# Optimization experiments

Measured on AMD Instinct MI355X. Metric: run time of the kernel, lower is better.

## Reference

```python
import jax, jax.numpy as jnp
import numpy as np

D = 64          # embedding_dim
B = 1024        # batch (queries)
R = 128         # num_relations
N = 100000      # num_nodes
E = 6400000     # num_edges


def setup_inputs() -> dict:
    key = jax.random.key(0)
    ks = jax.random.split(key, 16)
    inp = {
        "relation_embeddings": jax.random.normal(ks[0], (B, R, D), dtype=jnp.float32),
        "query_rels": jax.random.randint(ks[1], (B,), 0, R),
        "query_entities": jax.random.randint(ks[2], (B,), 0, N),
        "edge_index": jax.random.randint(ks[3], (2, E), 0, N),
        "edge_type": jax.random.randint(ks[4], (E,), 0, R),
        "num_nodes": N,
        # feature_extractor: Linear(2D+4 -> D), ReLU, Linear(D -> D//2), ReLU
        "W1": jax.random.normal(ks[5], (2 * D + 4, D), dtype=jnp.float32) * 0.05,
        "b1": jnp.zeros((D,), dtype=jnp.float32),
        "W2": jax.random.normal(ks[6], (D, D // 2), dtype=jnp.float32) * 0.05,
        "b2": jnp.zeros((D // 2,), dtype=jnp.float32),
        # gate_network: Linear(D//2 -> D//4), ReLU, Linear(D//4 -> 1), Sigmoid
        "Wg1": jax.random.normal(ks[7], (D // 2, D // 4), dtype=jnp.float32) * 0.05,
        "bg1": jnp.zeros((D // 4,), dtype=jnp.float32),
        "Wg2": jax.random.normal(ks[8], (D // 4, 1), dtype=jnp.float32) * 0.05,
        "bg2": jnp.full((1,), 0.85, dtype=jnp.float32),
    }
    return inp


def reference(relation_embeddings, query_rels, query_entities, edge_index,
              edge_type, num_nodes, W1, b1, W2, b2, Wg1, bg1, Wg2, bg2):
    b, r, d = relation_embeddings.shape
    e = edge_type.shape[0]
    e_f = jnp.float32(e)
    src, dst = edge_index[0], edge_index[1]
    # count self-loop edges once (matches boolean OR mask in torch code)
    not_loop = (src != dst).astype(jnp.float32)

    # --- graph statistics (vectorized replacement of per-query masks) ---
    rel_counts = jnp.zeros((r,), jnp.float32).at[edge_type].add(1.0)          # [R]
    rel_freq_norm = jnp.minimum(rel_counts[query_rels] / e_f, 1.0)            # [B]

    deg = (jnp.zeros((num_nodes,), jnp.float32)
           .at[src].add(1.0).at[dst].add(not_loop))                           # [N]
    deg_q = deg[query_entities]                                               # [B]
    entity_degree_norm = jnp.minimum(deg_q / e_f, 1.0)

    density = jnp.minimum(e_f / jnp.float32(num_nodes * num_nodes), 1.0)
    stats = jnp.stack([rel_freq_norm, entity_degree_norm, rel_freq_norm,
                       jnp.full_like(rel_freq_norm, density)], axis=-1)       # [B,4]

    # --- query relation embedding ---
    rel_emb = relation_embeddings[jnp.arange(b), query_rels]                  # [B,D]

    # --- entity embedding = mean of relation embeddings over incident edges ---
    # per-node histogram of incident edge types (self loops counted once)
    hist = (jnp.zeros((num_nodes, r), jnp.float32)
            .at[src, edge_type].add(1.0)
            .at[dst, edge_type].add(not_loop))                                # [N,R]
    Mq = hist[query_entities]                                                 # [B,R]
    ent_sum = jnp.einsum('br,brd->bd', Mq, relation_embeddings)               # [B,D]
    entity_emb = ent_sum / jnp.maximum(deg_q, 1.0)[:, None]                   # zeros if deg==0

    # --- gated MLP ---
    feat = jnp.concatenate([rel_emb, entity_emb, stats], axis=-1)             # [B,2D+4]
    h = jax.nn.relu(feat @ W1 + b1)
    h = jax.nn.relu(h @ W2 + b2)
    g = jax.nn.relu(h @ Wg1 + bg1)
    gate = jax.nn.sigmoid(g @ Wg2 + bg2)[:, 0]                                # [B]
    return gate
```

## Files before the change

kernel.cpp:

```cpp
#include <hip/hip_runtime.h>
#include <math.h>


#define NNODES 100000
#define NWORDS ((NNODES + 31) / 32)
#define NWP    (((NWORDS + 3) / 4) * 4)
#define RR     128
#define DD     64
#define FF     (2 * DD + 4)
#define E4C    1600000
#define EDGE_BLOCKS 512
#define NTC    (EDGE_BLOCKS * 1024)
#define HITCAP 2048
#define SETUP_BLOCKS 256

__global__ void __launch_bounds__(1024)
setup_kernel(const int* __restrict__ qents, int B,
             unsigned* __restrict__ gmask, int* __restrict__ gbase,
             const int* __restrict__ etype, int E,
             int* __restrict__ relcnt)
{
    int t = threadIdx.x;
    if (blockIdx.x != 0) {
        __shared__ int s_cnt[RR];
        if (t < RR) s_cnt[t] = 0;
        __syncthreads();
        int ne4 = E >> 2;
        const int4* et4 = (const int4*)etype;
        int i = (blockIdx.x - 1) * 1024 + t;
        int stride = (SETUP_BLOCKS - 1) * 1024;
        for (int k = i; k < ne4; k += stride) {
            int4 ty = et4[k];
            atomicAdd(&s_cnt[ty.x], 1);
            atomicAdd(&s_cnt[ty.y], 1);
            atomicAdd(&s_cnt[ty.z], 1);
            atomicAdd(&s_cnt[ty.w], 1);
        }
        if (blockIdx.x == 1) {
            for (int e = (ne4 << 2) + t; e < E; e += 1024)
                atomicAdd(&s_cnt[etype[e]], 1);
        }
        __syncthreads();
        if (t < RR) {
            int c = s_cnt[t];
            if (c) atomicAdd(&relcnt[t], c);
        }
        return;
    }
    __shared__ unsigned s_mask[NWP];
    __shared__ int s_wsum[16], s_wbase[16];
    for (int k = t; k < NWP; k += 1024) s_mask[k] = 0u;
    __syncthreads();
    for (int b = t; b < B; b += 1024) {
        int e = qents[b];
        atomicOr(&s_mask[e >> 5], 1u << (e & 31));
    }
    __syncthreads();
    int w0 = t * 4;
    int pc[4]; int sum = 0;
#pragma unroll
    for (int k = 0; k < 4; ++k) {
        int w = w0 + k;
        unsigned mm = (w < NWP) ? s_mask[w] : 0u;
        pc[k] = __popc(mm);
        sum += pc[k];
    }
    int lane = t & 63, wid = t >> 6;
    int incl = sum;
#pragma unroll
    for (int off = 1; off < 64; off <<= 1) {
        int v = __shfl_up(incl, off);
        if (lane >= off) incl += v;
    }
    if (lane == 63) s_wsum[wid] = incl;
    __syncthreads();
    if (t == 0) {
        int run = 0;
#pragma unroll
        for (int k = 0; k < 16; ++k) { s_wbase[k] = run; run += s_wsum[k]; }
    }
    __syncthreads();
    int base = s_wbase[wid] + incl - sum;
#pragma unroll
    for (int k = 0; k < 4; ++k) {
        int w = w0 + k;
        if (w < NWP) gbase[w] = base;
        base += pc[k];
    }
    for (int k = t; k < NWP; k += 1024) gmask[k] = s_mask[k];
}

static __device__ __forceinline__ void hitrec(
    int node, int e,
    const unsigned* s_mask, const int* s_base,
    unsigned short* s_hslot, unsigned* s_hedge, int* s_hn,
    int* __restrict__ Mslot, const int* __restrict__ etype)
{
    unsigned w = s_mask[node >> 5];
    if ((w >> (node & 31)) & 1u) {
        int slot = s_base[node >> 5] + __popc(w & ((1u << (node & 31)) - 1u));
        int idx = atomicAdd(s_hn, 1);
        if (idx < HITCAP) {
            s_hslot[idx] = (unsigned short)slot;
            s_hedge[idx] = (unsigned)e;
        } else {
            atomicAdd(&Mslot[slot * RR + etype[e]], 1);
        }
    }
}

static __device__ __forceinline__ void edge4s(
    int4 s, int4 d, int i,
    const unsigned* s_mask, const int* s_base,
    unsigned short* s_hslot, unsigned* s_hedge, int* s_hn,
    int* __restrict__ Mslot, const int* __restrict__ etype)
{
    int e = i * 4;
    hitrec(s.x, e + 0, s_mask, s_base, s_hslot, s_hedge, s_hn, Mslot, etype);
    if (s.x != d.x) hitrec(d.x, e + 0, s_mask, s_base, s_hslot, s_hedge, s_hn, Mslot, etype);
    hitrec(s.y, e + 1, s_mask, s_base, s_hslot, s_hedge, s_hn, Mslot, etype);
    if (s.y != d.y) hitrec(d.y, e + 1, s_mask, s_base, s_hslot, s_hedge, s_hn, Mslot, etype);
    hitrec(s.z, e + 2, s_mask, s_base, s_hslot, s_hedge, s_hn, Mslot, etype);
    if (s.z != d.z) hitrec(d.z, e + 2, s_mask, s_base, s_hslot, s_hedge, s_hn, Mslot, etype);
    hitrec(s.w, e + 3, s_mask, s_base, s_hslot, s_hedge, s_hn, Mslot, etype);
    if (s.w != d.w) hitrec(d.w, e + 3, s_mask, s_base, s_hslot, s_hedge, s_hn, Mslot, etype);
}

static __device__ __forceinline__ void edge1g(
    int s, int d, int ty,
    const unsigned* s_mask, const int* s_base, int* __restrict__ Mslot)
{
    unsigned ws = s_mask[s >> 5];
    if ((ws >> (s & 31)) & 1u) {
        int slot = s_base[s >> 5] + __popc(ws & ((1u << (s & 31)) - 1u));
        atomicAdd(&Mslot[slot * RR + ty], 1);
    }
    if (s != d) {
        unsigned wd = s_mask[d >> 5];
        if ((wd >> (d & 31)) & 1u) {
            int slot = s_base[d >> 5] + __popc(wd & ((1u << (d & 31)) - 1u));
            atomicAdd(&Mslot[slot * RR + ty], 1);
        }
    }
}

__global__ void __launch_bounds__(1024, 8)
edge_kernel(const int* __restrict__ ei, const int* __restrict__ etype,
            int E, int E4,
            const unsigned* __restrict__ gmask, const int* __restrict__ gbase,
            int* __restrict__ Mslot)
{
    __shared__ __align__(16) unsigned s_mask[NWP];
    __shared__ __align__(16) int s_base[NWP];
    __shared__ unsigned s_hedge[HITCAP];
    __shared__ unsigned short s_hslot[HITCAP];
    __shared__ int s_hn;
    int t = threadIdx.x;
    if (t == 0) s_hn = 0;
    const uint4* gm4 = (const uint4*)gmask;
    const int4*  gb4 = (const int4*)gbase;
    for (int i = t; i < NWP / 4; i += 1024) {
        ((uint4*)s_mask)[i] = gm4[i];
        ((int4*)s_base)[i]  = gb4[i];
    }
    __syncthreads();

    int tid  = blockIdx.x * 1024 + t;
    int nthr = gridDim.x * 1024;

    const int4* src4 = (const int4*)ei;
    const int4* dst4 = (const int4*)(ei + E);

    if (E4 == E4C && nthr == NTC) {
        int i0 = tid, i1 = tid + NTC, i2 = tid + 2 * NTC;
        int4 sa = src4[i0], da = dst4[i0];
        int4 sb = src4[i1], db = dst4[i1];
        int4 sc = src4[i2], dc = dst4[i2];
        edge4s(sa, da, i0, s_mask, s_base, s_hslot, s_hedge, &s_hn, Mslot, etype);
        edge4s(sb, db, i1, s_mask, s_base, s_hslot, s_hedge, &s_hn, Mslot, etype);
        edge4s(sc, dc, i2, s_mask, s_base, s_hslot, s_hedge, &s_hn, Mslot, etype);
        int i3 = tid + 3 * NTC;
        if (i3 < E4C) {
            int4 sd = src4[i3], dd = dst4[i3];
            edge4s(sd, dd, i3, s_mask, s_base, s_hslot, s_hedge, &s_hn, Mslot, etype);
        }
    } else {
        const int4* et4 = (const int4*)etype;
        for (int i = tid; i < E4; i += nthr) {
            int4 s = src4[i], d = dst4[i], ty = et4[i];
            edge1g(s.x, d.x, ty.x, s_mask, s_base, Mslot);
            edge1g(s.y, d.y, ty.y, s_mask, s_base, Mslot);
            edge1g(s.z, d.z, ty.z, s_mask, s_base, Mslot);
            edge1g(s.w, d.w, ty.w, s_mask, s_base, Mslot);
        }
        for (int e = (E4 << 2) + tid; e < E; e += nthr)
            edge1g(ei[e], ei[E + e], etype[e], s_mask, s_base, Mslot);
    }

    __syncthreads();
    int hn = s_hn; if (hn > HITCAP) hn = HITCAP;
    for (int i = t; i < hn; i += 1024) {
        int e  = (int)s_hedge[i];
        int ty = etype[e];
        atomicAdd(&Mslot[(int)s_hslot[i] * RR + ty], 1);
    }
}

__global__ void query_kernel(
    const float* __restrict__ RE,
    const int* __restrict__ qrels, const int* __restrict__ qents,
    const int* __restrict__ relcnt, const int* __restrict__ Mslot,
    const unsigned* __restrict__ gmask, const int* __restrict__ gbase,
    const float* __restrict__ W1, const float* __restrict__ b1,
    const float* __restrict__ W2, const float* __restrict__ b2,
    const float* __restrict__ Wg1, const float* __restrict__ bg1,
    const float* __restrict__ Wg2, const float* __restrict__ bg2,
    float* __restrict__ out, float e_f, float density)
{
    __shared__ float s_m[RR];
    __shared__ float s_part[256];
    __shared__ float s_feat[FF];
    __shared__ float s_h1[DD];
    __shared__ float s_h2[DD / 2];
    __shared__ float s_g[DD / 4];
    __shared__ int s_slot;

    int b = blockIdx.x;
    int t = threadIdx.x;
    int d = t & (DD - 1);
    int w = t >> 6;

    if (t == 0) {
        int e = qents[b];
        unsigned mm = gmask[e >> 5];
        s_slot = gbase[e >> 5] + __popc(mm & ((1u << (e & 31)) - 1u));
    }
    __syncthreads();
    int slot = s_slot;

    if (t < RR) s_m[t] = (float)Mslot[slot * RR + t];
    __syncthreads();

    const float* REb = RE + (size_t)b * RR * DD;
    float acc = 0.f;
#pragma unroll 4
    for (int r = w; r < RR; r += 4) {
        float m = s_m[r];
        if (m != 0.f) acc = fmaf(m, REb[r * DD + d], acc);
    }
    s_part[w * DD + d] = acc;
    __syncthreads();

    if (t < DD) {
        float ds = s_m[t] + s_m[t + DD];
#pragma unroll
        for (int off = 32; off > 0; off >>= 1) ds += __shfl_xor(ds, off);

        float ent = s_part[t] + s_part[DD + t] + s_part[2 * DD + t] + s_part[3 * DD + t];

        int qr = qrels[b];
        s_feat[t]      = REb[qr * DD + t];
        s_feat[DD + t] = ent / fmaxf(ds, 1.f);
        if (t == 0) {
            float rf = fminf((float)relcnt[qr] / e_f, 1.f);
            s_feat[2 * DD + 0] = rf;
            s_feat[2 * DD + 1] = fminf(ds / e_f, 1.f);
            s_feat[2 * DD + 2] = rf;
            s_feat[2 * DD + 3] = density;
        }
    }
    __syncthreads();

    {
        int c = t >> 6, n = t & 63;
        int i0 = c * 33;
        float a = 0.f;
#pragma unroll
        for (int k = 0; k < 33; ++k) {
            int i = i0 + k;
            a = fmaf(s_feat[i], W1[i * DD + n], a);
        }
        s_part[t] = a;
    }
    __syncthreads();
    if (t < DD) {
        float a = b1[t] + s_part[t] + s_part[64 + t] + s_part[128 + t] + s_part[192 + t];
        s_h1[t] = fmaxf(a, 0.f);
    }
    __syncthreads();

    {
        int c = t >> 5, n = t & 31;
        float a = 0.f;
#pragma unroll
        for (int k = 0; k < 8; ++k) {
            int i = c * 8 + k;
            a = fmaf(s_h1[i], W2[i * 32 + n], a);
        }
        s_part[t] = a;
    }
    __syncthreads();
    if (t < 32) {
        float a = b2[t];
#pragma unroll
        for (int c = 0; c < 8; ++c) a += s_part[c * 32 + t];
        s_h2[t] = fmaxf(a, 0.f);
    }
    __syncthreads();

    if (t < 16) {
        float a = bg1[t];
#pragma unroll
        for (int i = 0; i < 32; ++i) a = fmaf(s_h2[i], Wg1[i * 16 + t], a);
        s_g[t] = fmaxf(a, 0.f);
    }
    __syncthreads();

    if (t == 0) {
        float a = bg2[0];
#pragma unroll
        for (int i = 0; i < 16; ++i) a = fmaf(s_g[i], Wg2[i], a);
        out[b] = 1.f / (1.f + expf(-a));
    }
}

extern "C" void kernel_launch(void* const* d_in, const int* in_sizes, int n_in,
                              void* d_out, int out_size, void* d_ws, size_t ws_size,
                              hipStream_t stream)
{
    const float* RE    = (const float*)d_in[0];
    const int*   qrels = (const int*)d_in[1];
    const int*   qents = (const int*)d_in[2];
    const int*   ei    = (const int*)d_in[3];
    const int*   etype = (const int*)d_in[4];
    const float* W1  = (const float*)d_in[6];
    const float* b1  = (const float*)d_in[7];
    const float* W2  = (const float*)d_in[8];
    const float* b2  = (const float*)d_in[9];
    const float* Wg1 = (const float*)d_in[10];
    const float* bg1 = (const float*)d_in[11];
    const float* Wg2 = (const float*)d_in[12];
    const float* bg2 = (const float*)d_in[13];
    float* out = (float*)d_out;

    int B = in_sizes[1];
    int E = in_sizes[4];

    int* ws_i   = (int*)d_ws;
    int* Mslot  = ws_i;
    int* relcnt = Mslot + (size_t)B * RR;
    unsigned* mask = (unsigned*)(relcnt + RR);
    int* word_base = (int*)(mask + NWP);

    float e_f = (float)E;
    float density = fminf((float)E / ((float)NNODES * (float)NNODES), 1.f);

    hipMemsetAsync(d_ws, 0, ((size_t)B * RR + RR) * sizeof(int), stream);

    setup_kernel<<<SETUP_BLOCKS, 1024, 0, stream>>>(qents, B, mask, word_base,
                                                    etype, E, relcnt);

    int E4 = ((E & 3) == 0) ? (E >> 2) : 0;
    edge_kernel<<<EDGE_BLOCKS, 1024, 0, stream>>>(ei, etype, E, E4,
                                                  mask, word_base, Mslot);

    query_kernel<<<B, 256, 0, stream>>>(RE, qrels, qents, relcnt, Mslot,
                                        mask, word_base,
                                        W1, b1, W2, b2, Wg1, bg1, Wg2, bg2,
                                        out, e_f, density);
}
```

Baseline: 46.03 us.

## Shrink edge kernel LDS footprint and use smaller blocks for higher occupancy

The edge kernel drops its shared copy of the per-word base array and stores hit node ids instead of precomputed slots. Slots are now computed from global gbase only when a hit is flushed. Blocks go from 1024 to 256 threads with a smaller hit buffer, so more blocks can be resident per CU. The generic path now reuses the hit-buffer routine, the memset becomes a zero kernel, and the query kernel's zero-skip branch is removed with more unrolling. In exchange, hits pay extra global reads of gbase and the buffer overflows more easily into direct global atomics.

```diff
diff --git a/kernel.cpp b/kernel.cpp
--- a/kernel.cpp
+++ b/kernel.cpp
@@ -9,10 +9,19 @@
 #define DD     64
 #define FF     (2 * DD + 4)
 #define E4C    1600000
-#define EDGE_BLOCKS 512
-#define NTC    (EDGE_BLOCKS * 1024)
-#define HITCAP 2048
+#define EDGE_BLOCKS 2048
+#define EDGE_THREADS 256
+#define NTC    (EDGE_BLOCKS * EDGE_THREADS)
+#define HITCAP 512
 #define SETUP_BLOCKS 256
+
+__global__ void zero_kernel(int4* __restrict__ p, int n4)
+{
+    int i = blockIdx.x * blockDim.x + threadIdx.x;
+    int stride = gridDim.x * blockDim.x;
+    int4 z = make_int4(0, 0, 0, 0);
+    for (int k = i; k < n4; k += stride) p[k] = z;
+}
 
 __global__ void __launch_bounds__(1024)
 setup_kernel(const int* __restrict__ qents, int B,
@@ -92,18 +101,18 @@
 
 static __device__ __forceinline__ void hitrec(
     int node, int e,
-    const unsigned* s_mask, const int* s_base,
-    unsigned short* s_hslot, unsigned* s_hedge, int* s_hn,
+    const unsigned* s_mask, const int* __restrict__ gbase,
+    unsigned* s_hnode, unsigned* s_hedge, int* s_hn,
     int* __restrict__ Mslot, const int* __restrict__ etype)
 {
     unsigned w = s_mask[node >> 5];
     if ((w >> (node & 31)) & 1u) {
-        int slot = s_base[node >> 5] + __popc(w & ((1u << (node & 31)) - 1u));
         int idx = atomicAdd(s_hn, 1);
         if (idx < HITCAP) {
-            s_hslot[idx] = (unsigned short)slot;
+            s_hnode[idx] = (unsigned)node;
             s_hedge[idx] = (unsigned)e;
         } else {
+            int slot = gbase[node >> 5] + __popc(w & ((1u << (node & 31)) - 1u));
             atomicAdd(&Mslot[slot * RR + etype[e]], 1);
         }
     }
@@ -111,62 +120,40 @@
 
 static __device__ __forceinline__ void edge4s(
     int4 s, int4 d, int i,
-    const unsigned* s_mask, const int* s_base,
-    unsigned short* s_hslot, unsigned* s_hedge, int* s_hn,
+    const unsigned* s_mask, const int* __restrict__ gbase,
+    unsigned* s_hnode, unsigned* s_hedge, int* s_hn,
     int* __restrict__ Mslot, const int* __restrict__ etype)
 {
     int e = i * 4;
-    hitrec(s.x, e + 0, s_mask, s_base, s_hslot, s_hedge, s_hn, Mslot, etype);
-    if (s.x != d.x) hitrec(d.x, e + 0, s_mask, s_base, s_hslot, s_hedge, s_hn, Mslot, etype);
-    hitrec(s.y, e + 1, s_mask, s_base, s_hslot, s_hedge, s_hn, Mslot, etype);
-    if (s.y != d.y) hitrec(d.y, e + 1, s_mask, s_base, s_hslot, s_hedge, s_hn, Mslot, etype);
-    hitrec(s.z, e + 2, s_mask, s_base, s_hslot, s_hedge, s_hn, Mslot, etype);
-    if (s.z != d.z) hitrec(d.z, e + 2, s_mask, s_base, s_hslot, s_hedge, s_hn, Mslot, etype);
-    hitrec(s.w, e + 3, s_mask, s_base, s_hslot, s_hedge, s_hn, Mslot, etype);
-    if (s.w != d.w) hitrec(d.w, e + 3, s_mask, s_base, s_hslot, s_hedge, s_hn, Mslot, etype);
-}
-
-static __device__ __forceinline__ void edge1g(
-    int s, int d, int ty,
-    const unsigned* s_mask, const int* s_base, int* __restrict__ Mslot)
-{
-    unsigned ws = s_mask[s >> 5];
-    if ((ws >> (s & 31)) & 1u) {
-        int slot = s_base[s >> 5] + __popc(ws & ((1u << (s & 31)) - 1u));
-        atomicAdd(&Mslot[slot * RR + ty], 1);
-    }
-    if (s != d) {
-        unsigned wd = s_mask[d >> 5];
-        if ((wd >> (d & 31)) & 1u) {
-            int slot = s_base[d >> 5] + __popc(wd & ((1u << (d & 31)) - 1u));
-            atomicAdd(&Mslot[slot * RR + ty], 1);
-        }
-    }
-}
-
-__global__ void __launch_bounds__(1024, 8)
+    hitrec(s.x, e + 0, s_mask, gbase, s_hnode, s_hedge, s_hn, Mslot, etype);
+    if (s.x != d.x) hitrec(d.x, e + 0, s_mask, gbase, s_hnode, s_hedge, s_hn, Mslot, etype);
+    hitrec(s.y, e + 1, s_mask, gbase, s_hnode, s_hedge, s_hn, Mslot, etype);
+    if (s.y != d.y) hitrec(d.y, e + 1, s_mask, gbase, s_hnode, s_hedge, s_hn, Mslot, etype);
+    hitrec(s.z, e + 2, s_mask, gbase, s_hnode, s_hedge, s_hn, Mslot, etype);
+    if (s.z != d.z) hitrec(d.z, e + 2, s_mask, gbase, s_hnode, s_hedge, s_hn, Mslot, etype);
+    hitrec(s.w, e + 3, s_mask, gbase, s_hnode, s_hedge, s_hn, Mslot, etype);
+    if (s.w != d.w) hitrec(d.w, e + 3, s_mask, gbase, s_hnode, s_hedge, s_hn, Mslot, etype);
+}
+
+__global__ void __launch_bounds__(EDGE_THREADS, 8)
 edge_kernel(const int* __restrict__ ei, const int* __restrict__ etype,
             int E, int E4,
             const unsigned* __restrict__ gmask, const int* __restrict__ gbase,
             int* __restrict__ Mslot)
 {
     __shared__ __align__(16) unsigned s_mask[NWP];
-    __shared__ __align__(16) int s_base[NWP];
+    __shared__ unsigned s_hnode[HITCAP];
     __shared__ unsigned s_hedge[HITCAP];
-    __shared__ unsigned short s_hslot[HITCAP];
     __shared__ int s_hn;
     int t = threadIdx.x;
     if (t == 0) s_hn = 0;
     const uint4* gm4 = (const uint4*)gmask;
-    const int4*  gb4 = (const int4*)gbase;
-    for (int i = t; i < NWP / 4; i += 1024) {
+    for (int i = t; i < NWP / 4; i += EDGE_THREADS)
         ((uint4*)s_mask)[i] = gm4[i];
-        ((int4*)s_base)[i]  = gb4[i];
-    }
-    __syncthreads();
-
-    int tid  = blockIdx.x * 1024 + t;
-    int nthr = gridDim.x * 1024;
+    __syncthreads();
+
+    int tid  = blockIdx.x * EDGE_THREADS + t;
+    int nthr = gridDim.x * EDGE_THREADS;
 
     const int4* src4 = (const int4*)ei;
     const int4* dst4 = (const int4*)(ei + E);
@@ -176,33 +163,35 @@
         int4 sa = src4[i0], da = dst4[i0];
         int4 sb = src4[i1], db = dst4[i1];
         int4 sc = src4[i2], dc = dst4[i2];
-        edge4s(sa, da, i0, s_mask, s_base, s_hslot, s_hedge, &s_hn, Mslot, etype);
-        edge4s(sb, db, i1, s_mask, s_base, s_hslot, s_hedge, &s_hn, Mslot, etype);
-        edge4s(sc, dc, i2, s_mask, s_base, s_hslot, s_hedge, &s_hn, Mslot, etype);
+        edge4s(sa, da, i0, s_mask, gbase, s_hnode, s_hedge, &s_hn, Mslot, etype);
+        edge4s(sb, db, i1, s_mask, gbase, s_hnode, s_hedge, &s_hn, Mslot, etype);
+        edge4s(sc, dc, i2, s_mask, gbase, s_hnode, s_hedge, &s_hn, Mslot, etype);
         int i3 = tid + 3 * NTC;
         if (i3 < E4C) {
             int4 sd = src4[i3], dd = dst4[i3];
-            edge4s(sd, dd, i3, s_mask, s_base, s_hslot, s_hedge, &s_hn, Mslot, etype);
+            edge4s(sd, dd, i3, s_mask, gbase, s_hnode, s_hedge, &s_hn, Mslot, etype);
         }
     } else {
-        const int4* et4 = (const int4*)etype;
         for (int i = tid; i < E4; i += nthr) {
-            int4 s = src4[i], d = dst4[i], ty = et4[i];
-            edge1g(s.x, d.x, ty.x, s_mask, s_base, Mslot);
-            edge1g(s.y, d.y, ty.y, s_mask, s_base, Mslot);
-            edge1g(s.z, d.z, ty.z, s_mask, s_base, Mslot);
-            edge1g(s.w, d.w, ty.w, s_mask, s_base, Mslot);
-        }
-        for (int e = (E4 << 2) + tid; e < E; e += nthr)
-            edge1g(ei[e], ei[E + e], etype[e], s_mask, s_base, Mslot);
+            int4 s = src4[i], d = dst4[i];
+            edge4s(s, d, i, s_mask, gbase, s_hnode, s_hedge, &s_hn, Mslot, etype);
+        }
+        for (int e = (E4 << 2) + tid; e < E; e += nthr) {
+            int s = ei[e], d = ei[E + e];
+            hitrec(s, e, s_mask, gbase, s_hnode, s_hedge, &s_hn, Mslot, etype);
+            if (s != d)
+                hitrec(d, e, s_mask, gbase, s_hnode, s_hedge, &s_hn, Mslot, etype);
+        }
     }
 
     __syncthreads();
     int hn = s_hn; if (hn > HITCAP) hn = HITCAP;
-    for (int i = t; i < hn; i += 1024) {
-        int e  = (int)s_hedge[i];
-        int ty = etype[e];
-        atomicAdd(&Mslot[(int)s_hslot[i] * RR + ty], 1);
+    for (int i = t; i < hn; i += EDGE_THREADS) {
+        int node = (int)s_hnode[i];
+        int e    = (int)s_hedge[i];
+        unsigned w = s_mask[node >> 5];
+        int slot = gbase[node >> 5] + __popc(w & ((1u << (node & 31)) - 1u));
+        atomicAdd(&Mslot[slot * RR + etype[e]], 1);
     }
 }
 
@@ -243,11 +232,9 @@
 
     const float* REb = RE + (size_t)b * RR * DD;
     float acc = 0.f;
-#pragma unroll 4
-    for (int r = w; r < RR; r += 4) {
-        float m = s_m[r];
-        if (m != 0.f) acc = fmaf(m, REb[r * DD + d], acc);
-    }
+#pragma unroll 8
+    for (int r = w; r < RR; r += 4)
+        acc = fmaf(s_m[r], REb[r * DD + d], acc);
     s_part[w * DD + d] = acc;
     __syncthreads();
 
@@ -355,14 +342,15 @@
     float e_f = (float)E;
     float density = fminf((float)E / ((float)NNODES * (float)NNODES), 1.f);
 
-    hipMemsetAsync(d_ws, 0, ((size_t)B * RR + RR) * sizeof(int), stream);
+    int n4 = (B * RR + RR) / 4;
+    zero_kernel<<<256, 256, 0, stream>>>((int4*)d_ws, n4);
 
     setup_kernel<<<SETUP_BLOCKS, 1024, 0, stream>>>(qents, B, mask, word_base,
                                                     etype, E, relcnt);
 
     int E4 = ((E & 3) == 0) ? (E >> 2) : 0;
-    edge_kernel<<<EDGE_BLOCKS, 1024, 0, stream>>>(ei, etype, E, E4,
-                                                  mask, word_base, Mslot);
+    edge_kernel<<<EDGE_BLOCKS, EDGE_THREADS, 0, stream>>>(ei, etype, E, E4,
+                                                          mask, word_base, Mslot);
 
     query_kernel<<<B, 256, 0, stream>>>(RE, qrels, qents, relcnt, Mslot,
                                         mask, word_base,
```

Measured after the change: 44.56 us. 1.03x faster.
